# Kernel tuning notes

Hardware: AMD Instinct MI355X
Metric: run time of the kernel (lower is better)

The kernel has to match this reference:

```python
import jax, jax.numpy as jnp
import numpy as np


def setup_inputs() -> dict:
    B, C, D = 8192, 2048, 1024
    key = jax.random.key(0)
    kx, kc = jax.random.split(key)
    x = jax.random.normal(kx, (B, D), dtype=jnp.float32)
    # kaiming_normal_ init for centers: std = sqrt(2 / fan_in) with fan_in = feat_dim
    centers = jax.random.normal(kc, (C, D), dtype=jnp.float32) * jnp.sqrt(2.0 / D)
    sigma = jnp.ones((C, D), dtype=jnp.float32)  # nn.init.ones_
    return {"x": x, "centers": centers, "sigma": sigma}


def reference(x, centers, sigma):
    # Original loop computes, per class i:
    #   dist[:, i] = diag(m @ diag(sigma[i]) @ m.T)  with m = x - centers[i]
    # which equals sum_d sigma[i,d] * (x[b,d] - centers[i,d])^2.
    # Expand the square to avoid the O(B*C*D) broadcast intermediate:
    #   dist[b,i] = (x^2) @ sigma[i] - 2 * x @ (sigma[i]*centers[i]) + sum_d sigma[i,d]*centers[i,d]^2
    xsq_term = jnp.einsum('bd,id->bi', x * x, sigma)            # [B, C]
    cross = jnp.einsum('bd,id->bi', x, sigma * centers)          # [B, C]
    const = jnp.sum(sigma * centers * centers, axis=-1)          # [C]
    dist = xsq_term - 2.0 * cross + const[None, :]
    return (centers, sigma, -dist)
```

## Files before the change

kernel.cpp:

```cpp
#include <hip/hip_runtime.h>
#include <hip/hip_bf16.h>


#define B_SZ 8192
#define C_SZ 2048
#define D_SZ 1024
#define K2   2048

typedef __attribute__((ext_vector_type(4))) float f32x4;
typedef __attribute__((ext_vector_type(8))) short bf16x8;

static __device__ __forceinline__ unsigned short f2bf(float f) {
  union { float f; unsigned int u; } v; v.f = f;
  unsigned int r = v.u + 0x7fffu + ((v.u >> 16) & 1u);
  return (unsigned short)(r >> 16);
}

__global__ __launch_bounds__(256) void build_a(const float* __restrict__ x,
                                               unsigned short* __restrict__ Aop) {
  const long t = (long)blockIdx.x * 256 + threadIdx.x;
  const long e = t * 8;
  const long b = e >> 10;
  const int  d = (int)(e & 1023);
  const float4* xv = (const float4*)x;
  float4 v0 = xv[2 * t], v1 = xv[2 * t + 1];
  float vs[8] = {v0.x, v0.y, v0.z, v0.w, v1.x, v1.y, v1.z, v1.w};
  unsigned short sq[8] __attribute__((aligned(16)));
  unsigned short rw[8] __attribute__((aligned(16)));
#pragma unroll
  for (int j = 0; j < 8; ++j) {
    rw[j] = f2bf(vs[j]);
    sq[j] = f2bf(vs[j] * vs[j]);
  }
  *(uint4*)(Aop + b * K2 + d)        = *(uint4*)sq;
  *(uint4*)(Aop + b * K2 + D_SZ + d) = *(uint4*)rw;
}

__global__ __launch_bounds__(128) void prep_w(const float* __restrict__ centers,
                                              const float* __restrict__ sigma,
                                              float* __restrict__ out_centers,
                                              float* __restrict__ out_sigma,
                                              unsigned short* __restrict__ Wop,
                                              float* __restrict__ cn) {
  const int i = blockIdx.x;
  const int t = threadIdx.x;
  const long base = (long)i * D_SZ;
  const float4* cv = (const float4*)(centers + base);
  const float4* sv = (const float4*)(sigma + base);
  float4 c0 = cv[2 * t], c1 = cv[2 * t + 1];
  float4 s0 = sv[2 * t], s1 = sv[2 * t + 1];
  ((float4*)(out_centers + base))[2 * t]     = c0;
  ((float4*)(out_centers + base))[2 * t + 1] = c1;
  ((float4*)(out_sigma + base))[2 * t]       = s0;
  ((float4*)(out_sigma + base))[2 * t + 1]   = s1;
  float cs[8] = {c0.x, c0.y, c0.z, c0.w, c1.x, c1.y, c1.z, c1.w};
  float ss[8] = {s0.x, s0.y, s0.z, s0.w, s1.x, s1.y, s1.z, s1.w};
  unsigned short w1[8] __attribute__((aligned(16)));
  unsigned short w2[8] __attribute__((aligned(16)));
  float p = 0.0f;
#pragma unroll
  for (int j = 0; j < 8; ++j) {
    w1[j] = f2bf(-ss[j]);
    w2[j] = f2bf(2.0f * ss[j] * cs[j]);
    p += ss[j] * cs[j] * cs[j];
  }
  *(uint4*)(Wop + (long)i * K2 + t * 8)        = *(uint4*)w1;
  *(uint4*)(Wop + (long)i * K2 + D_SZ + t * 8) = *(uint4*)w2;
#pragma unroll
  for (int off = 32; off > 0; off >>= 1) p += __shfl_down(p, off, 64);
  __shared__ float red[2];
  if ((t & 63) == 0) red[t >> 6] = p;
  __syncthreads();
  if (t == 0) cn[i] = -(red[0] + red[1]);
}

#define VM6()  asm volatile("s_waitcnt vmcnt(6)" ::: "memory")
#define VM2()  asm volatile("s_waitcnt vmcnt(2)" ::: "memory")
#define VM0()  asm volatile("s_waitcnt vmcnt(0)" ::: "memory")
#define NOW()  ((void)0)
#define SB()   __builtin_amdgcn_sched_barrier(0)
#define BAR()  __builtin_amdgcn_s_barrier()

#define STAGE_A(C, KT)                                                          \
  do {                                                                          \
    __builtin_amdgcn_global_load_lds(                                           \
        (__attribute__((address_space(1))) void*)(aS + 0 * 64 * (long)K2 + (long)(KT) * 64), \
        (__attribute__((address_space(3))) void*)(&As[C][0 * 4096 + dstE]), 16, 0, 0);       \
    __builtin_amdgcn_global_load_lds(                                           \
        (__attribute__((address_space(1))) void*)(aS + 1 * 64 * (long)K2 + (long)(KT) * 64), \
        (__attribute__((address_space(3))) void*)(&As[C][1 * 4096 + dstE]), 16, 0, 0);       \
    __builtin_amdgcn_global_load_lds(                                           \
        (__attribute__((address_space(1))) void*)(aS + 2 * 64 * (long)K2 + (long)(KT) * 64), \
        (__attribute__((address_space(3))) void*)(&As[C][2 * 4096 + dstE]), 16, 0, 0);       \
    __builtin_amdgcn_global_load_lds(                                           \
        (__attribute__((address_space(1))) void*)(aS + 3 * 64 * (long)K2 + (long)(KT) * 64), \
        (__attribute__((address_space(3))) void*)(&As[C][3 * 4096 + dstE]), 16, 0, 0);       \
  } while (0)

#define STAGE_B(C, KT, KK)                                                      \
  do {                                                                          \
    __builtin_amdgcn_global_load_lds(                                           \
        (__attribute__((address_space(1))) void*)(bS + 0 * 128 * (long)K2 + (long)(KT) * 64 + (KK) * 32), \
        (__attribute__((address_space(3))) void*)(&Bs[C][0 * 4096 + dstE]), 16, 0, 0);                    \
    __builtin_amdgcn_global_load_lds(                                           \
        (__attribute__((address_space(1))) void*)(bS + 1 * 128 * (long)K2 + (long)(KT) * 64 + (KK) * 32), \
        (__attribute__((address_space(3))) void*)(&Bs[C][1 * 4096 + dstE]), 16, 0, 0);                    \
  } while (0)

#define LDA(BUF, KX, MI) (*(const bf16x8*)(&As[BUF][(aAddr ^ ((KX) * 32)) + (MI) * 1024]))
#define LDB(BUF, NI)     (*(const bf16x8*)(&Bs[BUF][bAddr + (NI) * 512]))

#define MM32(A0, A1, A2, A3, A4, A5, A6, A7, B0, B1, B2, B3)                     \
  acc[0][0] = __builtin_amdgcn_mfma_f32_16x16x32_bf16(A0, B0, acc[0][0], 0,0,0); \
  acc[0][1] = __builtin_amdgcn_mfma_f32_16x16x32_bf16(A0, B1, acc[0][1], 0,0,0); \
  acc[0][2] = __builtin_amdgcn_mfma_f32_16x16x32_bf16(A0, B2, acc[0][2], 0,0,0); \
  acc[0][3] = __builtin_amdgcn_mfma_f32_16x16x32_bf16(A0, B3, acc[0][3], 0,0,0); \
  acc[1][0] = __builtin_amdgcn_mfma_f32_16x16x32_bf16(A1, B0, acc[1][0], 0,0,0); \
  acc[1][1] = __builtin_amdgcn_mfma_f32_16x16x32_bf16(A1, B1, acc[1][1], 0,0,0); \
  acc[1][2] = __builtin_amdgcn_mfma_f32_16x16x32_bf16(A1, B2, acc[1][2], 0,0,0); \
  acc[1][3] = __builtin_amdgcn_mfma_f32_16x16x32_bf16(A1, B3, acc[1][3], 0,0,0); \
  acc[2][0] = __builtin_amdgcn_mfma_f32_16x16x32_bf16(A2, B0, acc[2][0], 0,0,0); \
  acc[2][1] = __builtin_amdgcn_mfma_f32_16x16x32_bf16(A2, B1, acc[2][1], 0,0,0); \
  acc[2][2] = __builtin_amdgcn_mfma_f32_16x16x32_bf16(A2, B2, acc[2][2], 0,0,0); \
  acc[2][3] = __builtin_amdgcn_mfma_f32_16x16x32_bf16(A2, B3, acc[2][3], 0,0,0); \
  acc[3][0] = __builtin_amdgcn_mfma_f32_16x16x32_bf16(A3, B0, acc[3][0], 0,0,0); \
  acc[3][1] = __builtin_amdgcn_mfma_f32_16x16x32_bf16(A3, B1, acc[3][1], 0,0,0); \
  acc[3][2] = __builtin_amdgcn_mfma_f32_16x16x32_bf16(A3, B2, acc[3][2], 0,0,0); \
  acc[3][3] = __builtin_amdgcn_mfma_f32_16x16x32_bf16(A3, B3, acc[3][3], 0,0,0); \
  acc[4][0] = __builtin_amdgcn_mfma_f32_16x16x32_bf16(A4, B0, acc[4][0], 0,0,0); \
  acc[4][1] = __builtin_amdgcn_mfma_f32_16x16x32_bf16(A4, B1, acc[4][1], 0,0,0); \
  acc[4][2] = __builtin_amdgcn_mfma_f32_16x16x32_bf16(A4, B2, acc[4][2], 0,0,0); \
  acc[4][3] = __builtin_amdgcn_mfma_f32_16x16x32_bf16(A4, B3, acc[4][3], 0,0,0); \
  acc[5][0] = __builtin_amdgcn_mfma_f32_16x16x32_bf16(A5, B0, acc[5][0], 0,0,0); \
  acc[5][1] = __builtin_amdgcn_mfma_f32_16x16x32_bf16(A5, B1, acc[5][1], 0,0,0); \
  acc[5][2] = __builtin_amdgcn_mfma_f32_16x16x32_bf16(A5, B2, acc[5][2], 0,0,0); \
  acc[5][3] = __builtin_amdgcn_mfma_f32_16x16x32_bf16(A5, B3, acc[5][3], 0,0,0); \
  acc[6][0] = __builtin_amdgcn_mfma_f32_16x16x32_bf16(A6, B0, acc[6][0], 0,0,0); \
  acc[6][1] = __builtin_amdgcn_mfma_f32_16x16x32_bf16(A6, B1, acc[6][1], 0,0,0); \
  acc[6][2] = __builtin_amdgcn_mfma_f32_16x16x32_bf16(A6, B2, acc[6][2], 0,0,0); \
  acc[6][3] = __builtin_amdgcn_mfma_f32_16x16x32_bf16(A6, B3, acc[6][3], 0,0,0); \
  acc[7][0] = __builtin_amdgcn_mfma_f32_16x16x32_bf16(A7, B0, acc[7][0], 0,0,0); \
  acc[7][1] = __builtin_amdgcn_mfma_f32_16x16x32_bf16(A7, B1, acc[7][1], 0,0,0); \
  acc[7][2] = __builtin_amdgcn_mfma_f32_16x16x32_bf16(A7, B2, acc[7][2], 0,0,0); \
  acc[7][3] = __builtin_amdgcn_mfma_f32_16x16x32_bf16(A7, B3, acc[7][3], 0,0,0);

#define TILE(AC, AN, AST, P1, P2, BS0, BS1, U, STGA, SB0_, SB1_, W0, W1, PRE)  \
  {                                                                   \
    if (SB0_) STAGE_B(BS0, (U) + 1, 1);                                        \
    if (STGA) STAGE_A(AST, (U) + 2);                                           \
    aQ0 = LDA(AC, 1, 0); aQ1 = LDA(AC, 1, 1);                                  \
    aQ2 = LDA(AC, 1, 2); aQ3 = LDA(AC, 1, 3);                                  \
    aQ4 = LDA(AC, 1, 4); aQ5 = LDA(AC, 1, 5);                                  \
    aQ6 = LDA(AC, 1, 6); aQ7 = LDA(AC, 1, 7);                                  \
    bQ0 = LDB(P1, 0); bQ1 = LDB(P1, 1); bQ2 = LDB(P1, 2); bQ3 = LDB(P1, 3);    \
    MM32(aP0, aP1, aP2, aP3, aP4, aP5, aP6, aP7, bP0, bP1, bP2, bP3)           \
    SB(); W0(); SB(); BAR();                                                   \
  }                                                                            \
  {                                                                   \
    if (SB1_) STAGE_B(BS1, (U) + 2, 0);                                        \
    if (PRE) {                                                                 \
      aP0 = LDA(AN, 0, 0); aP1 = LDA(AN, 0, 1);                                \
      aP2 = LDA(AN, 0, 2); aP3 = LDA(AN, 0, 3);                                \
      aP4 = LDA(AN, 0, 4); aP5 = LDA(AN, 0, 5);                                \
      aP6 = LDA(AN, 0, 6); aP7 = LDA(AN, 0, 7);                                \
      bP0 = LDB(P2, 0); bP1 = LDB(P2, 1); bP2 = LDB(P2, 2); bP3 = LDB(P2, 3);  \
    }                                                                          \
    MM32(aQ0, aQ1, aQ2, aQ3, aQ4, aQ5, aQ6, aQ7, bQ0, bQ1, bQ2, bQ3)          \
    SB(); W1(); SB(); BAR();                                                   \
  }

__global__ __launch_bounds__(512, 2) void gemm256(const unsigned short* __restrict__ A,
                                                  const unsigned short* __restrict__ W,
                                                  const float* __restrict__ cn,
                                                  float* __restrict__ out) {
  __shared__ __attribute__((aligned(16))) unsigned short As[3][16384];
  __shared__ __attribute__((aligned(16))) unsigned short Bs[3][8192];

  const int tid  = threadIdx.x;
  const int lane = tid & 63;
  const int wave = tid >> 6;
  const int wr = wave >> 2;
  const int wc = wave & 3;

  const int bid = blockIdx.x;
  const int xcd = bid & 7, idx = bid >> 3;
  const long rowBase = (long)(xcd * 4 + (idx >> 3)) * 256;
  const long colBase = (long)(idx & 7) * 256;

  const int sr = tid >> 3;
  const int sl = (tid & 7) ^ (sr & 7);
  const unsigned short* aS = A + (rowBase + sr) * (long)K2 + sl * 8;
  const int br = tid >> 2;
  const int bl = ((tid & 3) - br) & 3;
  const unsigned short* bS = W + (colBase + br) * (long)K2 + bl * 8;
  const int dstE = tid * 8;

  const int l15 = lane & 15, l7 = lane & 7, q = lane >> 4;
  const int aAddr = (wr * 128 + l15) * 64 + ((q ^ l7) * 8);
  const int bAddr = (wc * 64 + l15) * 32 + (((q + l15) & 3) * 8);

  f32x4 acc[8][4];
#pragma unroll
  for (int i = 0; i < 8; ++i)
#pragma unroll
    for (int j = 0; j < 4; ++j) acc[i][j] = (f32x4){0.f, 0.f, 0.f, 0.f};

  bf16x8 aP0, aP1, aP2, aP3, aP4, aP5, aP6, aP7;
  bf16x8 aQ0, aQ1, aQ2, aQ3, aQ4, aQ5, aQ6, aQ7;
  bf16x8 bP0, bP1, bP2, bP3, bQ0, bQ1, bQ2, bQ3;

  STAGE_A(0, 0);
  STAGE_B(0, 0, 0);
  STAGE_B(1, 0, 1);
  STAGE_A(1, 1);
  STAGE_B(2, 1, 0);
  VM6(); SB(); BAR();
  aP0 = LDA(0, 0, 0); aP1 = LDA(0, 0, 1); aP2 = LDA(0, 0, 2); aP3 = LDA(0, 0, 3);
  aP4 = LDA(0, 0, 4); aP5 = LDA(0, 0, 5); aP6 = LDA(0, 0, 6); aP7 = LDA(0, 0, 7);
  bP0 = LDB(0, 0); bP1 = LDB(0, 1); bP2 = LDB(0, 2); bP3 = LDB(0, 3);

#pragma unroll 1
  for (int u = 0; u < 30; u += 3) {
    TILE(0, 1, 2, 1, 2, 0, 1, u + 0, 1, 1, 1, VM6, VM6, 1);
    TILE(1, 2, 0, 0, 1, 2, 0, u + 1, 1, 1, 1, VM6, VM6, 1);
    TILE(2, 0, 1, 2, 0, 1, 2, u + 2, 1, 1, 1, VM6, VM6, 1);
  }
  TILE(0, 1, 2, 1, 2, 0, 1, 30, 0, 1, 0, VM2, VM0, 1);
  TILE(1, 2, 0, 0, 1, 2, 0, 31, 0, 0, 0, NOW, NOW, 0);

  const int crow = (lane >> 4) * 4;
  const int ccol = lane & 15;
#pragma unroll
  for (int ni = 0; ni < 4; ++ni) {
    const long col = colBase + wc * 64 + ni * 16 + ccol;
    const float c = cn[col];
#pragma unroll
    for (int mi = 0; mi < 8; ++mi) {
      const long row = rowBase + wr * 128 + mi * 16 + crow;
      float* o = out + row * C_SZ + col;
#pragma unroll
      for (int j = 0; j < 4; ++j) o[(long)j * C_SZ] = acc[mi][ni][j] + c;
    }
  }
}

extern "C" void kernel_launch(void* const* d_in, const int* in_sizes, int n_in,
                              void* d_out, int out_size, void* d_ws, size_t ws_size,
                              hipStream_t stream) {
  const float* x       = (const float*)d_in[0];
  const float* centers = (const float*)d_in[1];
  const float* sigma   = (const float*)d_in[2];
  float* out = (float*)d_out;

  unsigned short* Aop = (unsigned short*)d_ws;
  unsigned short* Wop = Aop + (long)B_SZ * K2;
  float* cnp = (float*)(Wop + (long)C_SZ * K2);

  build_a<<<B_SZ * D_SZ / 8 / 256, 256, 0, stream>>>(x, Aop);
  prep_w<<<C_SZ, 128, 0, stream>>>(centers, sigma,
                                   out, out + (size_t)C_SZ * D_SZ, Wop, cnp);

  float* out2 = out + (size_t)2 * C_SZ * D_SZ;
  gemm256<<<256, 512, 0, stream>>>(Aop, Wop, cnp, out2);
}
```

Baseline: 85.83 us.

## Switch GEMM inner loop from 16x16x32 to 32x32x16 bf16 MFMA tiles

```diff
diff --git a/kernel.cpp b/kernel.cpp
--- a/kernel.cpp
+++ b/kernel.cpp
@@ -8,6 +8,7 @@
 #define K2   2048
 
 typedef __attribute__((ext_vector_type(4))) float f32x4;
+typedef __attribute__((ext_vector_type(16))) float f32x16;
 typedef __attribute__((ext_vector_type(8))) short bf16x8;
 
 static __device__ __forceinline__ unsigned short f2bf(float f) {
@@ -107,66 +108,66 @@
         (__attribute__((address_space(3))) void*)(&Bs[C][1 * 4096 + dstE]), 16, 0, 0);                    \
   } while (0)
 
-#define LDA(BUF, KX, MI) (*(const bf16x8*)(&As[BUF][(aAddr ^ ((KX) * 32)) + (MI) * 1024]))
-#define LDB(BUF, NI)     (*(const bf16x8*)(&Bs[BUF][bAddr + (NI) * 512]))
-
-#define MM32(A0, A1, A2, A3, A4, A5, A6, A7, B0, B1, B2, B3)                     \
-  acc[0][0] = __builtin_amdgcn_mfma_f32_16x16x32_bf16(A0, B0, acc[0][0], 0,0,0); \
-  acc[0][1] = __builtin_amdgcn_mfma_f32_16x16x32_bf16(A0, B1, acc[0][1], 0,0,0); \
-  acc[0][2] = __builtin_amdgcn_mfma_f32_16x16x32_bf16(A0, B2, acc[0][2], 0,0,0); \
-  acc[0][3] = __builtin_amdgcn_mfma_f32_16x16x32_bf16(A0, B3, acc[0][3], 0,0,0); \
-  acc[1][0] = __builtin_amdgcn_mfma_f32_16x16x32_bf16(A1, B0, acc[1][0], 0,0,0); \
-  acc[1][1] = __builtin_amdgcn_mfma_f32_16x16x32_bf16(A1, B1, acc[1][1], 0,0,0); \
-  acc[1][2] = __builtin_amdgcn_mfma_f32_16x16x32_bf16(A1, B2, acc[1][2], 0,0,0); \
-  acc[1][3] = __builtin_amdgcn_mfma_f32_16x16x32_bf16(A1, B3, acc[1][3], 0,0,0); \
-  acc[2][0] = __builtin_amdgcn_mfma_f32_16x16x32_bf16(A2, B0, acc[2][0], 0,0,0); \
-  acc[2][1] = __builtin_amdgcn_mfma_f32_16x16x32_bf16(A2, B1, acc[2][1], 0,0,0); \
-  acc[2][2] = __builtin_amdgcn_mfma_f32_16x16x32_bf16(A2, B2, acc[2][2], 0,0,0); \
-  acc[2][3] = __builtin_amdgcn_mfma_f32_16x16x32_bf16(A2, B3, acc[2][3], 0,0,0); \
-  acc[3][0] = __builtin_amdgcn_mfma_f32_16x16x32_bf16(A3, B0, acc[3][0], 0,0,0); \
-  acc[3][1] = __builtin_amdgcn_mfma_f32_16x16x32_bf16(A3, B1, acc[3][1], 0,0,0); \
-  acc[3][2] = __builtin_amdgcn_mfma_f32_16x16x32_bf16(A3, B2, acc[3][2], 0,0,0); \
-  acc[3][3] = __builtin_amdgcn_mfma_f32_16x16x32_bf16(A3, B3, acc[3][3], 0,0,0); \
-  acc[4][0] = __builtin_amdgcn_mfma_f32_16x16x32_bf16(A4, B0, acc[4][0], 0,0,0); \
-  acc[4][1] = __builtin_amdgcn_mfma_f32_16x16x32_bf16(A4, B1, acc[4][1], 0,0,0); \
-  acc[4][2] = __builtin_amdgcn_mfma_f32_16x16x32_bf16(A4, B2, acc[4][2], 0,0,0); \
-  acc[4][3] = __builtin_amdgcn_mfma_f32_16x16x32_bf16(A4, B3, acc[4][3], 0,0,0); \
-  acc[5][0] = __builtin_amdgcn_mfma_f32_16x16x32_bf16(A5, B0, acc[5][0], 0,0,0); \
-  acc[5][1] = __builtin_amdgcn_mfma_f32_16x16x32_bf16(A5, B1, acc[5][1], 0,0,0); \
-  acc[5][2] = __builtin_amdgcn_mfma_f32_16x16x32_bf16(A5, B2, acc[5][2], 0,0,0); \
-  acc[5][3] = __builtin_amdgcn_mfma_f32_16x16x32_bf16(A5, B3, acc[5][3], 0,0,0); \
-  acc[6][0] = __builtin_amdgcn_mfma_f32_16x16x32_bf16(A6, B0, acc[6][0], 0,0,0); \
-  acc[6][1] = __builtin_amdgcn_mfma_f32_16x16x32_bf16(A6, B1, acc[6][1], 0,0,0); \
-  acc[6][2] = __builtin_amdgcn_mfma_f32_16x16x32_bf16(A6, B2, acc[6][2], 0,0,0); \
-  acc[6][3] = __builtin_amdgcn_mfma_f32_16x16x32_bf16(A6, B3, acc[6][3], 0,0,0); \
-  acc[7][0] = __builtin_amdgcn_mfma_f32_16x16x32_bf16(A7, B0, acc[7][0], 0,0,0); \
-  acc[7][1] = __builtin_amdgcn_mfma_f32_16x16x32_bf16(A7, B1, acc[7][1], 0,0,0); \
-  acc[7][2] = __builtin_amdgcn_mfma_f32_16x16x32_bf16(A7, B2, acc[7][2], 0,0,0); \
-  acc[7][3] = __builtin_amdgcn_mfma_f32_16x16x32_bf16(A7, B3, acc[7][3], 0,0,0);
+#define LDA(BUF, KS, MI) (*(const bf16x8*)(&As[BUF][aBase + (MI) * 2048 + sA##KS]))
+#define LDB(BUF, J, NI)  (*(const bf16x8*)(&Bs[BUF][bBase + (NI) * 1024 + sB##J]))
+
+#define MFMA3216 __builtin_amdgcn_mfma_f32_32x32x16_bf16
+
+#define MM8(A0, A1, A2, A3, B0, B1)        \
+  ac0 = MFMA3216(A0, B0, ac0, 0, 0, 0);    \
+  ac1 = MFMA3216(A0, B1, ac1, 0, 0, 0);    \
+  ac2 = MFMA3216(A1, B0, ac2, 0, 0, 0);    \
+  ac3 = MFMA3216(A1, B1, ac3, 0, 0, 0);    \
+  ac4 = MFMA3216(A2, B0, ac4, 0, 0, 0);    \
+  ac5 = MFMA3216(A2, B1, ac5, 0, 0, 0);    \
+  ac6 = MFMA3216(A3, B0, ac6, 0, 0, 0);    \
+  ac7 = MFMA3216(A3, B1, ac7, 0, 0, 0);
 
 #define TILE(AC, AN, AST, P1, P2, BS0, BS1, U, STGA, SB0_, SB1_, W0, W1, PRE)  \
-  {                                                                   \
+  {                                                               \
     if (SB0_) STAGE_B(BS0, (U) + 1, 1);                                        \
     if (STGA) STAGE_A(AST, (U) + 2);                                           \
-    aQ0 = LDA(AC, 1, 0); aQ1 = LDA(AC, 1, 1);                                  \
-    aQ2 = LDA(AC, 1, 2); aQ3 = LDA(AC, 1, 3);                                  \
-    aQ4 = LDA(AC, 1, 4); aQ5 = LDA(AC, 1, 5);                                  \
-    aQ6 = LDA(AC, 1, 6); aQ7 = LDA(AC, 1, 7);                                  \
-    bQ0 = LDB(P1, 0); bQ1 = LDB(P1, 1); bQ2 = LDB(P1, 2); bQ3 = LDB(P1, 3);    \
-    MM32(aP0, aP1, aP2, aP3, aP4, aP5, aP6, aP7, bP0, bP1, bP2, bP3)           \
+    aQ0 = LDA(AC, 2, 0); aQ1 = LDA(AC, 2, 1);                                  \
+    aQ2 = LDA(AC, 2, 2); aQ3 = LDA(AC, 2, 3);                                  \
+    aQ4 = LDA(AC, 3, 0); aQ5 = LDA(AC, 3, 1);                                  \
+    aQ6 = LDA(AC, 3, 2); aQ7 = LDA(AC, 3, 3);                                  \
+    bQ0 = LDB(P1, 0, 0); bQ1 = LDB(P1, 0, 1);                                  \
+    bQ2 = LDB(P1, 1, 0); bQ3 = LDB(P1, 1, 1);                                  \
+    SB();                                                                      \
+    __builtin_amdgcn_s_setprio(1);                                             \
+    MM8(aP0, aP1, aP2, aP3, bP0, bP1)                                          \
+    MM8(aP4, aP5, aP6, aP7, bP2, bP3)                                          \
+    __builtin_amdgcn_s_setprio(0);                                             \
     SB(); W0(); SB(); BAR();                                                   \
   }                                                                            \
-  {                                                                   \
+  {                                                               \
     if (SB1_) STAGE_B(BS1, (U) + 2, 0);                                        \
     if (PRE) {                                                                 \
       aP0 = LDA(AN, 0, 0); aP1 = LDA(AN, 0, 1);                                \
       aP2 = LDA(AN, 0, 2); aP3 = LDA(AN, 0, 3);                                \
-      aP4 = LDA(AN, 0, 4); aP5 = LDA(AN, 0, 5);                                \
-      aP6 = LDA(AN, 0, 6); aP7 = LDA(AN, 0, 7);                                \
-      bP0 = LDB(P2, 0); bP1 = LDB(P2, 1); bP2 = LDB(P2, 2); bP3 = LDB(P2, 3);  \
+      aP4 = LDA(AN, 1, 0); aP5 = LDA(AN, 1, 1);                                \
+      aP6 = LDA(AN, 1, 2); aP7 = LDA(AN, 1, 3);                                \
+      bP0 = LDB(P2, 0, 0); bP1 = LDB(P2, 0, 1);                                \
+      bP2 = LDB(P2, 1, 0); bP3 = LDB(P2, 1, 1);                                \
     }                                                                          \
-    MM32(aQ0, aQ1, aQ2, aQ3, aQ4, aQ5, aQ6, aQ7, bQ0, bQ1, bQ2, bQ3)          \
+    SB();                                                                      \
+    __builtin_amdgcn_s_setprio(1);                                             \
+    MM8(aQ0, aQ1, aQ2, aQ3, bQ0, bQ1)                                          \
+    MM8(aQ4, aQ5, aQ6, aQ7, bQ2, bQ3)                                          \
+    __builtin_amdgcn_s_setprio(0);                                             \
     SB(); W1(); SB(); BAR();                                                   \
+  }
+
+#define Z16(V)                                                                 \
+  _Pragma("unroll") for (int z_ = 0; z_ < 16; ++z_) V[z_] = 0.0f;
+
+#define EPI(ACF, MI, NI)                                                       \
+  {                                                                            \
+    const long col = colBase + wc * 64 + (NI) * 32 + (lane & 31);              \
+    const float c = cn[col];                                                   \
+    float* o = out + (rowBase + wr * 128 + (MI) * 32 + 4 * q5) * (long)C_SZ + col; \
+    _Pragma("unroll") for (int rg = 0; rg < 16; ++rg)                          \
+        o[(long)((rg & 3) + 8 * (rg >> 2)) * C_SZ] = ACF[rg] + c;              \
   }
 
 __global__ __launch_bounds__(512, 2) void gemm256(const unsigned short* __restrict__ A,
@@ -191,19 +192,23 @@
   const int sl = (tid & 7) ^ (sr & 7);
   const unsigned short* aS = A + (rowBase + sr) * (long)K2 + sl * 8;
   const int br = tid >> 2;
-  const int bl = ((tid & 3) - br) & 3;
+  const int bl = ((tid & 3) - (tid >> 3)) & 3;
   const unsigned short* bS = W + (colBase + br) * (long)K2 + bl * 8;
   const int dstE = tid * 8;
 
-  const int l15 = lane & 15, l7 = lane & 7, q = lane >> 4;
-  const int aAddr = (wr * 128 + l15) * 64 + ((q ^ l7) * 8);
-  const int bAddr = (wc * 64 + l15) * 32 + (((q + l15) & 3) * 8);
-
-  f32x4 acc[8][4];
-#pragma unroll
-  for (int i = 0; i < 8; ++i)
-#pragma unroll
-    for (int j = 0; j < 4; ++j) acc[i][j] = (f32x4){0.f, 0.f, 0.f, 0.f};
+  const int l31 = lane & 31, l7 = lane & 7, q5 = lane >> 5;
+  const int rp  = (lane >> 1) & 3;
+  const int aBase = (wr * 128 + l31) * 64;
+  const int bBase = (wc * 64 + l31) * 32;
+  const int sA0 = ((0 + q5) ^ l7) * 8;
+  const int sA1 = ((2 + q5) ^ l7) * 8;
+  const int sA2 = ((4 + q5) ^ l7) * 8;
+  const int sA3 = ((6 + q5) ^ l7) * 8;
+  const int sB0 = ((q5 + rp) & 3) * 8;
+  const int sB1 = ((2 + q5 + rp) & 3) * 8;
+
+  f32x16 ac0, ac1, ac2, ac3, ac4, ac5, ac6, ac7;
+  Z16(ac0) Z16(ac1) Z16(ac2) Z16(ac3) Z16(ac4) Z16(ac5) Z16(ac6) Z16(ac7)
 
   bf16x8 aP0, aP1, aP2, aP3, aP4, aP5, aP6, aP7;
   bf16x8 aQ0, aQ1, aQ2, aQ3, aQ4, aQ5, aQ6, aQ7;
@@ -216,8 +221,8 @@
   STAGE_B(2, 1, 0);
   VM6(); SB(); BAR();
   aP0 = LDA(0, 0, 0); aP1 = LDA(0, 0, 1); aP2 = LDA(0, 0, 2); aP3 = LDA(0, 0, 3);
-  aP4 = LDA(0, 0, 4); aP5 = LDA(0, 0, 5); aP6 = LDA(0, 0, 6); aP7 = LDA(0, 0, 7);
-  bP0 = LDB(0, 0); bP1 = LDB(0, 1); bP2 = LDB(0, 2); bP3 = LDB(0, 3);
+  aP4 = LDA(0, 1, 0); aP5 = LDA(0, 1, 1); aP6 = LDA(0, 1, 2); aP7 = LDA(0, 1, 3);
+  bP0 = LDB(0, 0, 0); bP1 = LDB(0, 0, 1); bP2 = LDB(0, 1, 0); bP3 = LDB(0, 1, 1);
 
 #pragma unroll 1
   for (int u = 0; u < 30; u += 3) {
@@ -228,20 +233,10 @@
   TILE(0, 1, 2, 1, 2, 0, 1, 30, 0, 1, 0, VM2, VM0, 1);
   TILE(1, 2, 0, 0, 1, 2, 0, 31, 0, 0, 0, NOW, NOW, 0);
 
-  const int crow = (lane >> 4) * 4;
-  const int ccol = lane & 15;
-#pragma unroll
-  for (int ni = 0; ni < 4; ++ni) {
-    const long col = colBase + wc * 64 + ni * 16 + ccol;
-    const float c = cn[col];
-#pragma unroll
-    for (int mi = 0; mi < 8; ++mi) {
-      const long row = rowBase + wr * 128 + mi * 16 + crow;
-      float* o = out + row * C_SZ + col;
-#pragma unroll
-      for (int j = 0; j < 4; ++j) o[(long)j * C_SZ] = acc[mi][ni][j] + c;
-    }
-  }
+  EPI(ac0, 0, 0) EPI(ac1, 0, 1)
+  EPI(ac2, 1, 0) EPI(ac3, 1, 1)
+  EPI(ac4, 2, 0) EPI(ac5, 2, 1)
+  EPI(ac6, 3, 0) EPI(ac7, 3, 1)
 }
 
 extern "C" void kernel_launch(void* const* d_in, const int* in_sizes, int n_in,
```

Measured after the change: 102.3 us. 19.2% more time.

## Restructure GEMM main loop into four barrier-separated phases with priority boosts

Applied to the files above, without the earlier changes.

```diff
diff --git a/kernel.cpp b/kernel.cpp
--- a/kernel.cpp
+++ b/kernel.cpp
@@ -78,95 +78,92 @@
 #define VM2()  asm volatile("s_waitcnt vmcnt(2)" ::: "memory")
 #define VM0()  asm volatile("s_waitcnt vmcnt(0)" ::: "memory")
 #define NOW()  ((void)0)
+#define LGKM0() asm volatile("s_waitcnt lgkmcnt(0)" ::: "memory")
 #define SB()   __builtin_amdgcn_sched_barrier(0)
 #define BAR()  __builtin_amdgcn_s_barrier()
 
-#define STAGE_A(C, KT)                                                          \
+#define STAGE_A2(C, KT, H)                                                      \
   do {                                                                          \
     __builtin_amdgcn_global_load_lds(                                           \
-        (__attribute__((address_space(1))) void*)(aS + 0 * 64 * (long)K2 + (long)(KT) * 64), \
-        (__attribute__((address_space(3))) void*)(&As[C][0 * 4096 + dstE]), 16, 0, 0);       \
-    __builtin_amdgcn_global_load_lds(                                           \
-        (__attribute__((address_space(1))) void*)(aS + 1 * 64 * (long)K2 + (long)(KT) * 64), \
-        (__attribute__((address_space(3))) void*)(&As[C][1 * 4096 + dstE]), 16, 0, 0);       \
-    __builtin_amdgcn_global_load_lds(                                           \
-        (__attribute__((address_space(1))) void*)(aS + 2 * 64 * (long)K2 + (long)(KT) * 64), \
-        (__attribute__((address_space(3))) void*)(&As[C][2 * 4096 + dstE]), 16, 0, 0);       \
-    __builtin_amdgcn_global_load_lds(                                           \
-        (__attribute__((address_space(1))) void*)(aS + 3 * 64 * (long)K2 + (long)(KT) * 64), \
-        (__attribute__((address_space(3))) void*)(&As[C][3 * 4096 + dstE]), 16, 0, 0);       \
+        (__attribute__((address_space(1))) void*)(aS + ((H)*128 + 0) * (long)K2 + (long)(KT)*64),  \
+        (__attribute__((address_space(3))) void*)(&As[C][(H)*8192 + dstE]), 16, 0, 0);             \
+    __builtin_amdgcn_global_load_lds(                                           \
+        (__attribute__((address_space(1))) void*)(aS + ((H)*128 + 64) * (long)K2 + (long)(KT)*64), \
+        (__attribute__((address_space(3))) void*)(&As[C][(H)*8192 + 4096 + dstE]), 16, 0, 0);      \
   } while (0)
 
 #define STAGE_B(C, KT, KK)                                                      \
   do {                                                                          \
     __builtin_amdgcn_global_load_lds(                                           \
-        (__attribute__((address_space(1))) void*)(bS + 0 * 128 * (long)K2 + (long)(KT) * 64 + (KK) * 32), \
-        (__attribute__((address_space(3))) void*)(&Bs[C][0 * 4096 + dstE]), 16, 0, 0);                    \
-    __builtin_amdgcn_global_load_lds(                                           \
-        (__attribute__((address_space(1))) void*)(bS + 1 * 128 * (long)K2 + (long)(KT) * 64 + (KK) * 32), \
-        (__attribute__((address_space(3))) void*)(&Bs[C][1 * 4096 + dstE]), 16, 0, 0);                    \
+        (__attribute__((address_space(1))) void*)(bS + 0 * 128 * (long)K2 + (long)(KT)*64 + (KK)*32), \
+        (__attribute__((address_space(3))) void*)(&Bs[C][0 * 4096 + dstE]), 16, 0, 0);                \
+    __builtin_amdgcn_global_load_lds(                                           \
+        (__attribute__((address_space(1))) void*)(bS + 1 * 128 * (long)K2 + (long)(KT)*64 + (KK)*32), \
+        (__attribute__((address_space(3))) void*)(&Bs[C][1 * 4096 + dstE]), 16, 0, 0);                \
   } while (0)
 
 #define LDA(BUF, KX, MI) (*(const bf16x8*)(&As[BUF][(aAddr ^ ((KX) * 32)) + (MI) * 1024]))
 #define LDB(BUF, NI)     (*(const bf16x8*)(&Bs[BUF][bAddr + (NI) * 512]))
 
-#define MM32(A0, A1, A2, A3, A4, A5, A6, A7, B0, B1, B2, B3)                     \
-  acc[0][0] = __builtin_amdgcn_mfma_f32_16x16x32_bf16(A0, B0, acc[0][0], 0,0,0); \
-  acc[0][1] = __builtin_amdgcn_mfma_f32_16x16x32_bf16(A0, B1, acc[0][1], 0,0,0); \
-  acc[0][2] = __builtin_amdgcn_mfma_f32_16x16x32_bf16(A0, B2, acc[0][2], 0,0,0); \
-  acc[0][3] = __builtin_amdgcn_mfma_f32_16x16x32_bf16(A0, B3, acc[0][3], 0,0,0); \
-  acc[1][0] = __builtin_amdgcn_mfma_f32_16x16x32_bf16(A1, B0, acc[1][0], 0,0,0); \
-  acc[1][1] = __builtin_amdgcn_mfma_f32_16x16x32_bf16(A1, B1, acc[1][1], 0,0,0); \
-  acc[1][2] = __builtin_amdgcn_mfma_f32_16x16x32_bf16(A1, B2, acc[1][2], 0,0,0); \
-  acc[1][3] = __builtin_amdgcn_mfma_f32_16x16x32_bf16(A1, B3, acc[1][3], 0,0,0); \
-  acc[2][0] = __builtin_amdgcn_mfma_f32_16x16x32_bf16(A2, B0, acc[2][0], 0,0,0); \
-  acc[2][1] = __builtin_amdgcn_mfma_f32_16x16x32_bf16(A2, B1, acc[2][1], 0,0,0); \
-  acc[2][2] = __builtin_amdgcn_mfma_f32_16x16x32_bf16(A2, B2, acc[2][2], 0,0,0); \
-  acc[2][3] = __builtin_amdgcn_mfma_f32_16x16x32_bf16(A2, B3, acc[2][3], 0,0,0); \
-  acc[3][0] = __builtin_amdgcn_mfma_f32_16x16x32_bf16(A3, B0, acc[3][0], 0,0,0); \
-  acc[3][1] = __builtin_amdgcn_mfma_f32_16x16x32_bf16(A3, B1, acc[3][1], 0,0,0); \
-  acc[3][2] = __builtin_amdgcn_mfma_f32_16x16x32_bf16(A3, B2, acc[3][2], 0,0,0); \
-  acc[3][3] = __builtin_amdgcn_mfma_f32_16x16x32_bf16(A3, B3, acc[3][3], 0,0,0); \
-  acc[4][0] = __builtin_amdgcn_mfma_f32_16x16x32_bf16(A4, B0, acc[4][0], 0,0,0); \
-  acc[4][1] = __builtin_amdgcn_mfma_f32_16x16x32_bf16(A4, B1, acc[4][1], 0,0,0); \
-  acc[4][2] = __builtin_amdgcn_mfma_f32_16x16x32_bf16(A4, B2, acc[4][2], 0,0,0); \
-  acc[4][3] = __builtin_amdgcn_mfma_f32_16x16x32_bf16(A4, B3, acc[4][3], 0,0,0); \
-  acc[5][0] = __builtin_amdgcn_mfma_f32_16x16x32_bf16(A5, B0, acc[5][0], 0,0,0); \
-  acc[5][1] = __builtin_amdgcn_mfma_f32_16x16x32_bf16(A5, B1, acc[5][1], 0,0,0); \
-  acc[5][2] = __builtin_amdgcn_mfma_f32_16x16x32_bf16(A5, B2, acc[5][2], 0,0,0); \
-  acc[5][3] = __builtin_amdgcn_mfma_f32_16x16x32_bf16(A5, B3, acc[5][3], 0,0,0); \
-  acc[6][0] = __builtin_amdgcn_mfma_f32_16x16x32_bf16(A6, B0, acc[6][0], 0,0,0); \
-  acc[6][1] = __builtin_amdgcn_mfma_f32_16x16x32_bf16(A6, B1, acc[6][1], 0,0,0); \
-  acc[6][2] = __builtin_amdgcn_mfma_f32_16x16x32_bf16(A6, B2, acc[6][2], 0,0,0); \
-  acc[6][3] = __builtin_amdgcn_mfma_f32_16x16x32_bf16(A6, B3, acc[6][3], 0,0,0); \
-  acc[7][0] = __builtin_amdgcn_mfma_f32_16x16x32_bf16(A7, B0, acc[7][0], 0,0,0); \
-  acc[7][1] = __builtin_amdgcn_mfma_f32_16x16x32_bf16(A7, B1, acc[7][1], 0,0,0); \
-  acc[7][2] = __builtin_amdgcn_mfma_f32_16x16x32_bf16(A7, B2, acc[7][2], 0,0,0); \
-  acc[7][3] = __builtin_amdgcn_mfma_f32_16x16x32_bf16(A7, B3, acc[7][3], 0,0,0);
-
-#define TILE(AC, AN, AST, P1, P2, BS0, BS1, U, STGA, SB0_, SB1_, W0, W1, PRE)  \
-  {                                                                   \
-    if (SB0_) STAGE_B(BS0, (U) + 1, 1);                                        \
-    if (STGA) STAGE_A(AST, (U) + 2);                                           \
-    aQ0 = LDA(AC, 1, 0); aQ1 = LDA(AC, 1, 1);                                  \
-    aQ2 = LDA(AC, 1, 2); aQ3 = LDA(AC, 1, 3);                                  \
-    aQ4 = LDA(AC, 1, 4); aQ5 = LDA(AC, 1, 5);                                  \
-    aQ6 = LDA(AC, 1, 6); aQ7 = LDA(AC, 1, 7);                                  \
-    bQ0 = LDB(P1, 0); bQ1 = LDB(P1, 1); bQ2 = LDB(P1, 2); bQ3 = LDB(P1, 3);    \
-    MM32(aP0, aP1, aP2, aP3, aP4, aP5, aP6, aP7, bP0, bP1, bP2, bP3)           \
-    SB(); W0(); SB(); BAR();                                                   \
+#define MFMA16 __builtin_amdgcn_mfma_f32_16x16x32_bf16
+
+#define MM16(A0, A1, A2, A3, B0, B1, B2, B3, R)        \
+  acc[(R)+0][0] = MFMA16(A0, B0, acc[(R)+0][0], 0,0,0);\
+  acc[(R)+0][1] = MFMA16(A0, B1, acc[(R)+0][1], 0,0,0);\
+  acc[(R)+0][2] = MFMA16(A0, B2, acc[(R)+0][2], 0,0,0);\
+  acc[(R)+0][3] = MFMA16(A0, B3, acc[(R)+0][3], 0,0,0);\
+  acc[(R)+1][0] = MFMA16(A1, B0, acc[(R)+1][0], 0,0,0);\
+  acc[(R)+1][1] = MFMA16(A1, B1, acc[(R)+1][1], 0,0,0);\
+  acc[(R)+1][2] = MFMA16(A1, B2, acc[(R)+1][2], 0,0,0);\
+  acc[(R)+1][3] = MFMA16(A1, B3, acc[(R)+1][3], 0,0,0);\
+  acc[(R)+2][0] = MFMA16(A2, B0, acc[(R)+2][0], 0,0,0);\
+  acc[(R)+2][1] = MFMA16(A2, B1, acc[(R)+2][1], 0,0,0);\
+  acc[(R)+2][2] = MFMA16(A2, B2, acc[(R)+2][2], 0,0,0);\
+  acc[(R)+2][3] = MFMA16(A2, B3, acc[(R)+2][3], 0,0,0);\
+  acc[(R)+3][0] = MFMA16(A3, B0, acc[(R)+3][0], 0,0,0);\
+  acc[(R)+3][1] = MFMA16(A3, B1, acc[(R)+3][1], 0,0,0);\
+  acc[(R)+3][2] = MFMA16(A3, B2, acc[(R)+3][2], 0,0,0);\
+  acc[(R)+3][3] = MFMA16(A3, B3, acc[(R)+3][3], 0,0,0);
+
+#define PH_MID() BAR(); LGKM0(); SB(); __builtin_amdgcn_s_setprio(1)
+#define PH_END(WW) __builtin_amdgcn_s_setprio(0); SB(); WW(); SB(); BAR()
+
+#define TILE8(AC, AST, BH0, BH1, U, STGA, STGB1, STGB2, WB, WD)                \
+  {                                            \
+    aA0 = LDA(AC, 0, 0); aA1 = LDA(AC, 0, 1);                                  \
+    aA2 = LDA(AC, 0, 2); aA3 = LDA(AC, 0, 3);                                  \
+    bP0 = LDB(BH0, 0); bP1 = LDB(BH0, 1);                                      \
+    bP2 = LDB(BH0, 2); bP3 = LDB(BH0, 3);                                      \
+    if (STGA) STAGE_A2(AST, (U) + 2, 0);                                       \
+    PH_MID();                                                                  \
+    MM16(aA0, aA1, aA2, aA3, bP0, bP1, bP2, bP3, 0)                            \
+    PH_END(NOW);                                                               \
   }                                                                            \
-  {                                                                   \
-    if (SB1_) STAGE_B(BS1, (U) + 2, 0);                                        \
-    if (PRE) {                                                                 \
-      aP0 = LDA(AN, 0, 0); aP1 = LDA(AN, 0, 1);                                \
-      aP2 = LDA(AN, 0, 2); aP3 = LDA(AN, 0, 3);                                \
-      aP4 = LDA(AN, 0, 4); aP5 = LDA(AN, 0, 5);                                \
-      aP6 = LDA(AN, 0, 6); aP7 = LDA(AN, 0, 7);                                \
-      bP0 = LDB(P2, 0); bP1 = LDB(P2, 1); bP2 = LDB(P2, 2); bP3 = LDB(P2, 3);  \
-    }                                                                          \
-    MM32(aQ0, aQ1, aQ2, aQ3, aQ4, aQ5, aQ6, aQ7, bQ0, bQ1, bQ2, bQ3)          \
-    SB(); W1(); SB(); BAR();                                                   \
+  {                                            \
+    aB0 = LDA(AC, 0, 4); aB1 = LDA(AC, 0, 5);                                  \
+    aB2 = LDA(AC, 0, 6); aB3 = LDA(AC, 0, 7);                                  \
+    if (STGA) STAGE_A2(AST, (U) + 2, 1);                                       \
+    PH_MID();                                                                  \
+    MM16(aB0, aB1, aB2, aB3, bP0, bP1, bP2, bP3, 4)                            \
+    PH_END(WB);                                                                \
+  }                                                                            \
+  {                                            \
+    aA0 = LDA(AC, 1, 0); aA1 = LDA(AC, 1, 1);                                  \
+    aA2 = LDA(AC, 1, 2); aA3 = LDA(AC, 1, 3);                                  \
+    bQ0 = LDB(BH1, 0); bQ1 = LDB(BH1, 1);                                      \
+    bQ2 = LDB(BH1, 2); bQ3 = LDB(BH1, 3);                                      \
+    if (STGB1) STAGE_B(BH0, (U) + 1, 1);                                       \
+    PH_MID();                                                                  \
+    MM16(aA0, aA1, aA2, aA3, bQ0, bQ1, bQ2, bQ3, 0)                            \
+    PH_END(NOW);                                                               \
+  }                                                                            \
+  {                                            \
+    aB0 = LDA(AC, 1, 4); aB1 = LDA(AC, 1, 5);                                  \
+    aB2 = LDA(AC, 1, 6); aB3 = LDA(AC, 1, 7);                                  \
+    if (STGB2) STAGE_B(BH1, (U) + 2, 0);                                       \
+    PH_MID();                                                                  \
+    MM16(aB0, aB1, aB2, aB3, bQ0, bQ1, bQ2, bQ3, 4)                            \
+    PH_END(WD);                                                                \
   }
 
 __global__ __launch_bounds__(512, 2) void gemm256(const unsigned short* __restrict__ A,
@@ -191,13 +188,13 @@
   const int sl = (tid & 7) ^ (sr & 7);
   const unsigned short* aS = A + (rowBase + sr) * (long)K2 + sl * 8;
   const int br = tid >> 2;
-  const int bl = ((tid & 3) - br) & 3;
+  const int bl = ((tid & 3) - (tid >> 3)) & 3;
   const unsigned short* bS = W + (colBase + br) * (long)K2 + bl * 8;
   const int dstE = tid * 8;
 
   const int l15 = lane & 15, l7 = lane & 7, q = lane >> 4;
   const int aAddr = (wr * 128 + l15) * 64 + ((q ^ l7) * 8);
-  const int bAddr = (wc * 64 + l15) * 32 + (((q + l15) & 3) * 8);
+  const int bAddr = (wc * 64 + l15) * 32 + (((q + (l15 >> 1)) & 3) * 8);
 
   f32x4 acc[8][4];
 #pragma unroll
@@ -205,28 +202,24 @@
 #pragma unroll
     for (int j = 0; j < 4; ++j) acc[i][j] = (f32x4){0.f, 0.f, 0.f, 0.f};
 
-  bf16x8 aP0, aP1, aP2, aP3, aP4, aP5, aP6, aP7;
-  bf16x8 aQ0, aQ1, aQ2, aQ3, aQ4, aQ5, aQ6, aQ7;
+  bf16x8 aA0, aA1, aA2, aA3, aB0, aB1, aB2, aB3;
   bf16x8 bP0, bP1, bP2, bP3, bQ0, bQ1, bQ2, bQ3;
 
-  STAGE_A(0, 0);
+  STAGE_A2(0, 0, 0); STAGE_A2(0, 0, 1);
   STAGE_B(0, 0, 0);
+  STAGE_A2(1, 1, 0); STAGE_A2(1, 1, 1);
   STAGE_B(1, 0, 1);
-  STAGE_A(1, 1);
   STAGE_B(2, 1, 0);
   VM6(); SB(); BAR();
-  aP0 = LDA(0, 0, 0); aP1 = LDA(0, 0, 1); aP2 = LDA(0, 0, 2); aP3 = LDA(0, 0, 3);
-  aP4 = LDA(0, 0, 4); aP5 = LDA(0, 0, 5); aP6 = LDA(0, 0, 6); aP7 = LDA(0, 0, 7);
-  bP0 = LDB(0, 0); bP1 = LDB(0, 1); bP2 = LDB(0, 2); bP3 = LDB(0, 3);
 
 #pragma unroll 1
   for (int u = 0; u < 30; u += 3) {
-    TILE(0, 1, 2, 1, 2, 0, 1, u + 0, 1, 1, 1, VM6, VM6, 1);
-    TILE(1, 2, 0, 0, 1, 2, 0, u + 1, 1, 1, 1, VM6, VM6, 1);
-    TILE(2, 0, 1, 2, 0, 1, 2, u + 2, 1, 1, 1, VM6, VM6, 1);
-  }
-  TILE(0, 1, 2, 1, 2, 0, 1, 30, 0, 1, 0, VM2, VM0, 1);
-  TILE(1, 2, 0, 0, 1, 2, 0, 31, 0, 0, 0, NOW, NOW, 0);
+    TILE8(0, 2, 0, 1, u + 0, 1, 1, 1, VM6, VM6);
+    TILE8(1, 0, 2, 0, u + 1, 1, 1, 1, VM6, VM6);
+    TILE8(2, 1, 1, 2, u + 2, 1, 1, 1, VM6, VM6);
+  }
+  TILE8(0, 2, 0, 1, 30, 0, 1, 0, VM2, VM2);
+  TILE8(1, 0, 2, 0, 31, 0, 0, 0, VM0, NOW);
 
   const int crow = (lane >> 4) * 4;
   const int ccol = lane & 15;
```

After: 90.77 us. 1.06x slower.
